# Kernel optimization log

Measured on AMD Instinct MI355X. Metric: run time of the kernel, lower is better.

## Reference

```python
import jax, jax.numpy as jnp
import numpy as np

N = 100000        # nodes
E = 1600000       # edges (avg degree 16)
F_IN = 128        # in_features
AH = 16           # attention_size
ALPHA = 0.2       # LeakyReLU negative slope


def setup_inputs() -> dict:
    key = jax.random.key(0)
    ks = jax.random.split(key, 10)
    xav = lambda k, shp, fan: jax.random.normal(k, shp, jnp.float32) * (1.414 * (2.0 / fan) ** 0.5)
    return {
        "input": jax.random.normal(ks[0], (N, F_IN), jnp.float32),
        "edges": jax.random.randint(ks[1], (2, E), 0, N, jnp.int32),
        "edge_factor": jax.random.normal(ks[2], (E,), jnp.float32),
        "adj_sparse_sum_rowwise": jnp.ones((N, 1), jnp.float32),
        "degree": jax.random.uniform(ks[3], (N,), jnp.float32) + 0.1,
        # Linear_2mini: in_features -> attention_hid
        "w_mini": xav(ks[4], (F_IN, AH), F_IN + AH),
        "b_mini": jnp.zeros((AH,), jnp.float32),
        "attention_bias": jnp.zeros((1, AH), jnp.float32),
        # linear_factor1: 3*AH -> AH ; linear_factor2: AH -> 1
        "lf1_w": xav(ks[5], (3 * AH, AH), 4 * AH),
        "lf1_b": jnp.zeros((AH,), jnp.float32),
        "lf2_w": xav(ks[6], (AH, 1), AH + 1),
        "lf2_b": jnp.zeros((1,), jnp.float32),
        "adj": 0,
        "iftrain": 0,
    }


def _edge_mlp(h_src, h_dst, h_diff, lf1_w, lf1_b, lf2_w, lf2_b):
    # [E, 3*AH] -> [E, AH] -> leaky_relu -> [E, 1] -> sigmoid -> [E]
    f = jnp.concatenate([h_src, h_dst, h_diff], axis=1)
    f = f @ lf1_w + lf1_b
    f = jax.nn.leaky_relu(f, ALPHA)
    f = f @ lf2_w + lf2_b
    return jax.nn.sigmoid(f[:, 0])


def reference(input, edges, edge_factor, adj_sparse_sum_rowwise, degree,
              w_mini, b_mini, attention_bias, lf1_w, lf1_b, lf2_w, lf2_b,
              adj, iftrain):
    n = input.shape[0]
    src, dst = edges[0], edges[1]

    # Linear_2mini projection [N, AH]
    new_h_mini = input @ w_mini + b_mini
    h_src = new_h_mini[src]                   # [E, AH]
    h_dst = new_h_mini[dst]                   # [E, AH]
    h_diff = jnp.abs(h_dst - h_src)           # [E, AH]

    # first edge MLP -> sigmoid factor per edge
    fc0 = _edge_mlp(h_src, h_dst, h_diff, lf1_w, lf1_b, lf2_w, lf2_b)  # [E]

    # row-wise MEAN of fc0 over edges grouped by source row (spmm reduce='mean')
    row_cnt = jax.ops.segment_sum(jnp.ones_like(fc0), src, num_segments=n)
    factor_res_1hop = jax.ops.segment_sum(fc0, src, num_segments=n) / jnp.maximum(row_cnt, 1.0)  # [N]

    factor_src = factor_res_1hop[src]         # [E]
    factor_dst = factor_res_1hop[dst]         # [E]

    # second edge MLP with attention bias added to endpoints
    fc1 = _edge_mlp(h_src + attention_bias, h_dst + attention_bias, h_diff,
                    lf1_w, lf1_b, lf2_w, lf2_b)  # [E]

    ef = factor_src * factor_dst * fc1        # new edge_factor [E]

    # row-wise SUM of edge factors (spmm with ones, reduce='sum')
    ef_row_sum = jax.ops.segment_sum(ef, src, num_segments=n)[:, None]  # [N,1]
    aggr_factor = ef_row_sum / adj_sparse_sum_rowwise                   # [N,1]

    deg = degree[:, None]                                               # [N,1]
    # sparse matmul: out[i] = sum_{e: src[e]=i} ef[e] * (input*deg)[dst[e]]
    msg = ef[:, None] * (input * deg)[dst]                              # [E, F]
    spmm = jax.ops.segment_sum(msg, src, num_segments=n)                # [N, F]

    final_h = spmm * deg + (1.0 - aggr_factor) * input
    return final_h, ef
```

## Files before the change

### kernel.cpp

```cpp
#include <hip/hip_runtime.h>
#include <math.h>

#define F_IN 128
#define AH 16
#define ALPHA 0.2f
#define NB_MAX 1024
#define TILE 2048
#define EPT 8
#define CAP 5120
#define PCAP 6144

typedef __attribute__((ext_vector_type(8))) short short8;
typedef __attribute__((ext_vector_type(4))) float f32x4;
typedef __attribute__((ext_vector_type(2))) float f32x2;

__device__ __forceinline__ unsigned f2bf_rn(float x) {
    unsigned u = __float_as_uint(x);
    return (u + 0x7fffu + ((u >> 16) & 1u)) >> 16;
}
#define LOF(u) __uint_as_float((u) << 16)
#define HIF(u) __uint_as_float((u) & 0xffff0000u)

#if __has_builtin(__builtin_amdgcn_cvt_pk_fp8_f32) && __has_builtin(__builtin_amdgcn_cvt_pk_f32_fp8)
__device__ __forceinline__ unsigned short fp8_pack2(float x, float y) {
    return (unsigned short)(__builtin_amdgcn_cvt_pk_fp8_f32(x, y, 0, false) & 0xffff);
}
__device__ __forceinline__ f32x2 fp8_unpack2(unsigned short u) {
    return __builtin_amdgcn_cvt_pk_f32_fp8((int)(unsigned)u, false);
}
#else
__device__ __forceinline__ unsigned fp8_enc1(float x) {
    unsigned u = __float_as_uint(x);
    const unsigned s = (u >> 24) & 0x80u;
    u &= 0x7fffffffu;
    if (u < 0x3C000000u) return s;
    if (u < 0x3C800000u) return s | 0x08u;
    const unsigned r = u + 0x7ffffu + ((u >> 20) & 1u);
    const unsigned e32 = r >> 23;
    return s | (((e32 - 120u) & 0xfu) << 3) | ((r >> 20) & 7u);
}
__device__ __forceinline__ unsigned short fp8_pack2(float x, float y) {
    return (unsigned short)(fp8_enc1(x) | (fp8_enc1(y) << 8));
}
__device__ __forceinline__ float fp8_dec1(unsigned b) {
    return __uint_as_float(((b & 0x80u) << 24) | ((b & 0x7fu) << 20)) * 0x1p120f;
}
__device__ __forceinline__ f32x2 fp8_unpack2(unsigned short u) {
    f32x2 r; r.x = fp8_dec1((unsigned)u & 0xffu); r.y = fp8_dec1((unsigned)u >> 8);
    return r;
}
#endif


__global__ void k_mini(const float* __restrict__ input,
                       const float* __restrict__ w,
                       const float* __restrict__ b,
                       const float* __restrict__ degree,
                       unsigned short* __restrict__ hb,
                       unsigned short* __restrict__ simf8, int n) {
    __shared__ float ws[F_IN * AH];
    __shared__ float rows[16][F_IN + 1];
    __shared__ float dgs[16];
    for (int i = threadIdx.x; i < F_IN * AH; i += blockDim.x) ws[i] = w[i];
    const int base = blockIdx.x * 16;
    for (int idx = threadIdx.x; idx < 16 * F_IN; idx += blockDim.x) {
        const int l = idx >> 7, f = idx & 127;
        const int node = base + l;
        rows[l][f] = (node < n) ? input[(size_t)node * F_IN + f] : 0.f;
    }
    if (threadIdx.x < 16) {
        const int node = base + threadIdx.x;
        dgs[threadIdx.x] = (node < n) ? degree[node] : 0.f;
    }
    __syncthreads();
    {
        const int l = threadIdx.x >> 4;
        const int j = threadIdx.x & 15;
        const int node = base + l;
        if (node < n) {
            float acc = b[j];
            #pragma unroll 8
            for (int f = 0; f < F_IN; ++f) acc += rows[l][f] * ws[f * AH + j];
            hb[(size_t)node * AH + j] = (unsigned short)f2bf_rn(acc);
        }
    }
    for (int idx = threadIdx.x; idx < 16 * 64; idx += blockDim.x) {
        const int l = idx >> 6, pr = idx & 63;
        const int node = base + l;
        if (node < n) {
            const float dg = dgs[l];
            simf8[(size_t)node * 64 + pr] =
                fp8_pack2(rows[l][2 * pr] * dg, rows[l][2 * pr + 1] * dg);
        }
    }
}

__global__ void k_binit(int* __restrict__ bucket_cur, int nb1,
                        const float* __restrict__ lf1_w, const float* __restrict__ ab,
                        float* __restrict__ Cj) {
    for (int b = threadIdx.x; b < nb1; b += blockDim.x) bucket_cur[b] = b * CAP;
    if (threadIdx.x < AH) {
        float c = 0.f;
        for (int k = 0; k < AH; ++k)
            c += ab[k] * (lf1_w[k * AH + threadIdx.x] + lf1_w[(AH + k) * AH + threadIdx.x]);
        Cj[threadIdx.x] = c;
    }
}

__global__ __launch_bounds__(256, 4)
void k_mlp_part1(const int* __restrict__ src, const int* __restrict__ dst,
                 const unsigned short* __restrict__ hb,
                 const float* __restrict__ lf1_w, const float* __restrict__ lf1_b,
                 const float* __restrict__ lf2_w, const float* __restrict__ lf2_b,
                 const float* __restrict__ Cj,
                 unsigned* __restrict__ fcb,
                 int* __restrict__ bucket_cur,
                 unsigned long long* __restrict__ rec, int e, int nb1) {
    __shared__ unsigned lds_fc[TILE];
    __shared__ int lhist[NB_MAX];
    __shared__ int lbase[NB_MAX];
    const int t0   = blockIdx.x * TILE;
    const int lane = threadIdx.x & 63;
    const int wv   = threadIdx.x >> 6;
    const int g    = lane >> 4;
    const int col  = lane & 15;
    for (int k = threadIdx.x; k < nb1; k += 256) lhist[k] = 0;

    short8 A1, A2;
    #pragma unroll
    for (int i = 0; i < 8; ++i) {
        A1[i] = (short)f2bf_rn(lf1_w[(8 * g + i) * AH + col]);
        A2[i] = (g < 2) ? (short)f2bf_rn(lf1_w[(32 + 8 * g + i) * AH + col]) : (short)0;
    }
    const f32x4 bias4 = *(const f32x4*)(lf1_b + 4 * g);
    const f32x4 cj4   = *(const f32x4*)(Cj + 4 * g);
    const f32x4 w24   = *(const f32x4*)(lf2_w + 4 * g);
    const float b2    = lf2_b[0];

    const int CPW = TILE / 64;
    for (int c = wv * CPW; c < (wv + 1) * CPW; ++c) {
        const int eidx = t0 + c * 16 + col;
        const bool ev  = (eidx < e);
        const int s = ev ? src[eidx] : 0;
        const int d = ev ? dst[eidx] : 0;
        const int rowi = (g < 2) ? s : d;
        const uint4 B1u = *(const uint4*)(hb + (size_t)rowi * AH + (g & 1) * 8);
        uint4 H;
        H.x = (unsigned)__shfl_xor((int)B1u.x, 32);
        H.y = (unsigned)__shfl_xor((int)B1u.y, 32);
        H.z = (unsigned)__shfl_xor((int)B1u.z, 32);
        H.w = (unsigned)__shfl_xor((int)B1u.w, 32);
        uint4 B2u;
        B2u.x = (f2bf_rn(fabsf(HIF(H.x) - HIF(B1u.x))) << 16) | f2bf_rn(fabsf(LOF(H.x) - LOF(B1u.x)));
        B2u.y = (f2bf_rn(fabsf(HIF(H.y) - HIF(B1u.y))) << 16) | f2bf_rn(fabsf(LOF(H.y) - LOF(B1u.y)));
        B2u.z = (f2bf_rn(fabsf(HIF(H.z) - HIF(B1u.z))) << 16) | f2bf_rn(fabsf(LOF(H.z) - LOF(B1u.z)));
        B2u.w = (f2bf_rn(fabsf(HIF(H.w) - HIF(B1u.w))) << 16) | f2bf_rn(fabsf(LOF(H.w) - LOF(B1u.w)));

        f32x4 acc = bias4;
        acc = __builtin_amdgcn_mfma_f32_16x16x32_bf16(A1, *(const short8*)&B1u, acc, 0, 0, 0);
        acc = __builtin_amdgcn_mfma_f32_16x16x32_bf16(A2, *(const short8*)&B2u, acc, 0, 0, 0);

        float p0 = 0.f, p1 = 0.f;
        #pragma unroll
        for (int r = 0; r < 4; ++r) {
            const float f  = acc[r];
            const float v0 = f > 0.f ? f : ALPHA * f;
            const float t  = f + cj4[r];
            const float v1 = t > 0.f ? t : ALPHA * t;
            p0 += w24[r] * v0;
            p1 += w24[r] * v1;
        }
        p0 += __shfl_xor(p0, 16); p1 += __shfl_xor(p1, 16);
        p0 += __shfl_xor(p0, 32); p1 += __shfl_xor(p1, 32);
        if (lane < 16) {
            const float fc0 = 1.f / (1.f + expf(-(p0 + b2)));
            const float fc1 = 1.f / (1.f + expf(-(p1 + b2)));
            lds_fc[c * 16 + col] = (f2bf_rn(fc1) << 16) | f2bf_rn(fc0);
        }
    }
    __syncthreads();
    int sv[EPT], rv[EPT];
    #pragma unroll
    for (int k = 0; k < EPT; ++k) {
        const int i = t0 + k * 256 + threadIdx.x;
        if (i < e) {
            const int s = src[i];
            sv[k] = s;
            rv[k] = atomicAdd(&lhist[s >> 8], 1);
        } else { sv[k] = -1; rv[k] = 0; }
    }
    __syncthreads();
    for (int k = threadIdx.x; k < nb1; k += 256) {
        const int c = lhist[k];
        lbase[k] = c ? atomicAdd(&bucket_cur[k], c) : 0;
    }
    __syncthreads();
    #pragma unroll
    for (int k = 0; k < EPT; ++k) {
        const int i = t0 + k * 256 + threadIdx.x;
        if (i < e) {
            const int s = sv[k];
            const unsigned fc = lds_fc[i - t0];
            fcb[i] = fc;
            const unsigned lo = ((unsigned)(s & 255) << 24) | (unsigned)dst[i];
            rec[lbase[s >> 8] + rv[k]] = ((unsigned long long)fc << 32) | lo;
        }
    }
}

__global__ void k_bscan(const int* __restrict__ bucket_cur, int* __restrict__ base,
                        int nb1, int e) {
    __shared__ int sh[1024];
    const int t = threadIdx.x;
    const int v = (t < nb1) ? (bucket_cur[t] - t * CAP) : 0;
    sh[t] = v; __syncthreads();
    for (int off = 1; off < 1024; off <<= 1) {
        const int x = (t >= off) ? sh[t - off] : 0;
        __syncthreads();
        sh[t] += x;
        __syncthreads();
    }
    if (t < nb1) base[t] = sh[t] - v;
    if (t == nb1) base[t] = e;
}

__global__ __launch_bounds__(256)
void k_part2(const int* __restrict__ bucket_cur, const int* __restrict__ bucket_base,
             const unsigned long long* __restrict__ rec,
             unsigned long long* __restrict__ rec2,
             int* __restrict__ row_end, int* __restrict__ cnt,
             float* __restrict__ factor, int n) {
    __shared__ unsigned long long lds[PCAP];
    __shared__ int lcnt[256];
    __shared__ int sh[256];
    __shared__ float lsum[256];
    const int b = blockIdx.x;
    const int start = b * CAP;
    const int count = bucket_cur[b] - start;
    const int out0  = bucket_base[b];
    lcnt[threadIdx.x] = 0;
    lsum[threadIdx.x] = 0.f;
    __syncthreads();
    for (int k = threadIdx.x; k < count; k += 256) {
        const unsigned long long r = rec[start + k];
        if (k < PCAP) lds[k] = r;
        const int off = (int)(((unsigned)r >> 24) & 255u);
        atomicAdd(&lcnt[off], 1);
        atomicAdd(&lsum[off], __uint_as_float(((unsigned)(r >> 32) & 0xffffu) << 16));
    }
    __syncthreads();
    const int v = lcnt[threadIdx.x];
    sh[threadIdx.x] = v; __syncthreads();
    for (int off = 1; off < 256; off <<= 1) {
        const int x = (threadIdx.x >= off) ? sh[threadIdx.x - off] : 0;
        __syncthreads();
        sh[threadIdx.x] += x;
        __syncthreads();
    }
    const int inc = sh[threadIdx.x];
    const int node = (b << 8) + threadIdx.x;
    if (node < n) {
        row_end[node] = out0 + inc;
        cnt[node] = v;
        factor[node] = lsum[threadIdx.x] / fmaxf((float)v, 1.f);
    }
    lcnt[threadIdx.x] = inc - v;
    __syncthreads();
    for (int k = threadIdx.x; k < count; k += 256) {
        const unsigned long long r = (k < PCAP) ? lds[k] : rec[start + k];
        const int off = (int)(((unsigned)r >> 24) & 255u);
        const int p = out0 + atomicAdd(&lcnt[off], 1);
        rec2[p] = r;
    }
}

__global__ void k_ef(const int* __restrict__ src, const int* __restrict__ dst,
                     const unsigned* __restrict__ fcb, const float* __restrict__ factor,
                     float* __restrict__ ef_out, int e) {
    const int i = blockIdx.x * blockDim.x + threadIdx.x;
    if (i < e) {
        const unsigned fb = fcb[i];
        ef_out[i] = factor[src[i]] * factor[dst[i]] *
                    __uint_as_float(fb & 0xffff0000u);
    }
}

__global__ void k_spmm_final(const int* __restrict__ row_end, const int* __restrict__ cnt,
                             const unsigned long long* __restrict__ rec,
                             const float* __restrict__ factor,
                             const unsigned short* __restrict__ simf8,
                             const float* __restrict__ input,
                             const float* __restrict__ degree,
                             const float* __restrict__ adj_row,
                             float* __restrict__ out_h, int n) {
    __shared__ float2 sh[256];
    const int wid  = (blockIdx.x * blockDim.x + threadIdx.x) >> 6;
    const int lane = threadIdx.x & 63;
    const int sbase = threadIdx.x & ~63;
    if (wid >= n) return;
    const int end = row_end[wid];
    const int beg = end - cnt[wid];
    const float fnode = factor[wid];
    float acc0 = 0.f, acc1 = 0.f, efl = 0.f;
    for (int base = beg; base < end; base += 64) {
        const int rem = end - base;
        const int mm = rem < 64 ? rem : 64;
        float ef = 0.f; int dl = 0;
        if (lane < mm) {
            const unsigned long long r = rec[base + lane];
            const int d = (int)((unsigned)r & 0xffffffu);
            const float fc1 = __uint_as_float((unsigned)(r >> 32) & 0xffff0000u);
            ef = fnode * factor[d] * fc1;
            dl = d;
        }
        efl += ef;
        sh[sbase + lane] = make_float2(ef, __int_as_float(dl));
        for (int j = 0; j < mm; j += 8) {
            float2 t0 = sh[sbase + j + 0];
            float2 t1 = sh[sbase + j + 1];
            float2 t2 = sh[sbase + j + 2];
            float2 t3 = sh[sbase + j + 3];
            float2 t4 = sh[sbase + j + 4];
            float2 t5 = sh[sbase + j + 5];
            float2 t6 = sh[sbase + j + 6];
            float2 t7 = sh[sbase + j + 7];
            const unsigned short u0 = simf8[(size_t)__float_as_int(t0.y) * 64 + lane];
            const unsigned short u1 = simf8[(size_t)__float_as_int(t1.y) * 64 + lane];
            const unsigned short u2 = simf8[(size_t)__float_as_int(t2.y) * 64 + lane];
            const unsigned short u3 = simf8[(size_t)__float_as_int(t3.y) * 64 + lane];
            const unsigned short u4 = simf8[(size_t)__float_as_int(t4.y) * 64 + lane];
            const unsigned short u5 = simf8[(size_t)__float_as_int(t5.y) * 64 + lane];
            const unsigned short u6 = simf8[(size_t)__float_as_int(t6.y) * 64 + lane];
            const unsigned short u7 = simf8[(size_t)__float_as_int(t7.y) * 64 + lane];
            const f32x2 v0 = fp8_unpack2(u0);
            const f32x2 v1 = fp8_unpack2(u1);
            const f32x2 v2 = fp8_unpack2(u2);
            const f32x2 v3 = fp8_unpack2(u3);
            const f32x2 v4 = fp8_unpack2(u4);
            const f32x2 v5 = fp8_unpack2(u5);
            const f32x2 v6 = fp8_unpack2(u6);
            const f32x2 v7 = fp8_unpack2(u7);
            acc0 += t0.x * v0.x; acc1 += t0.x * v0.y;
            acc0 += t1.x * v1.x; acc1 += t1.x * v1.y;
            acc0 += t2.x * v2.x; acc1 += t2.x * v2.y;
            acc0 += t3.x * v3.x; acc1 += t3.x * v3.y;
            acc0 += t4.x * v4.x; acc1 += t4.x * v4.y;
            acc0 += t5.x * v5.x; acc1 += t5.x * v5.y;
            acc0 += t6.x * v6.x; acc1 += t6.x * v6.y;
            acc0 += t7.x * v7.x; acc1 += t7.x * v7.y;
        }
    }
    for (int off = 32; off > 0; off >>= 1) efl += __shfl_xor(efl, off);
    const float aggr = efl / adj_row[wid];
    const float dg = degree[wid];
    const float2 inn = *(const float2*)(input + (size_t)wid * F_IN + 2 * lane);
    float2 o;
    o.x = acc0 * dg + (1.f - aggr) * inn.x;
    o.y = acc1 * dg + (1.f - aggr) * inn.y;
    *(float2*)(out_h + (size_t)wid * F_IN + 2 * lane) = o;
}

extern "C" void kernel_launch(void* const* d_in, const int* in_sizes, int n_in,
                              void* d_out, int out_size, void* d_ws, size_t ws_size,
                              hipStream_t stream) {
    const float* input   = (const float*)d_in[0];
    const int*   edges   = (const int*)  d_in[1];
    const float* adj_row = (const float*)d_in[3];
    const float* degree  = (const float*)d_in[4];
    const float* w_mini  = (const float*)d_in[5];
    const float* b_mini  = (const float*)d_in[6];
    const float* ab      = (const float*)d_in[7];
    const float* lf1_w   = (const float*)d_in[8];
    const float* lf1_b   = (const float*)d_in[9];
    const float* lf2_w   = (const float*)d_in[10];
    const float* lf2_b   = (const float*)d_in[11];

    const int N = in_sizes[0] / F_IN;
    const int E = in_sizes[1] / 2;
    const int NB1 = (N + 255) >> 8;
    const int* src = edges;
    const int* dst = edges + E;

    float* final_h = (float*)d_out;
    float* ef_out  = (float*)d_out + (size_t)N * F_IN;

    unsigned short* hb  = (unsigned short*)d_ws;
    unsigned* fcb  = (unsigned*)(hb + (size_t)N * AH);
    float* factor  = (float*)(fcb + E);
    int*   cnt     = (int*)(factor + N);
    int*   row_end = cnt + N;
    float* Cj      = (float*)(row_end + N);
    int*   bucket_base = (int*)(Cj + 16);
    int*   bucket_cur  = bucket_base + NB_MAX + 1;
    unsigned long long* rec =
        (unsigned long long*)((((uintptr_t)(bucket_cur + NB_MAX)) + 15) & ~(uintptr_t)15);
    unsigned long long* rec2 = rec + (size_t)NB1 * CAP;
    unsigned short* simf8 =
        (unsigned short*)((((uintptr_t)(rec2 + E)) + 255) & ~(uintptr_t)255);

    k_mini<<<(N + 15) / 16, 256, 0, stream>>>(input, w_mini, b_mini, degree, hb, simf8, N);
    k_binit<<<1, 512, 0, stream>>>(bucket_cur, NB1, lf1_w, ab, Cj);
    k_mlp_part1<<<(E + TILE - 1) / TILE, 256, 0, stream>>>(src, dst, hb,
                                                           lf1_w, lf1_b, lf2_w, lf2_b, Cj,
                                                           fcb, bucket_cur, rec, E, NB1);
    k_bscan<<<1, 1024, 0, stream>>>(bucket_cur, bucket_base, NB1, E);
    k_part2<<<NB1, 256, 0, stream>>>(bucket_cur, bucket_base, rec, rec2,
                                     row_end, cnt, factor, N);
    k_ef<<<(E + 255) / 256, 256, 0, stream>>>(src, dst, fcb, factor, ef_out, E);
    k_spmm_final<<<(N * 64 + 255) / 256, 256, 0, stream>>>(row_end, cnt, rec2, factor, simf8,
                                                           input, degree, adj_row, final_h, N);
}
```

Baseline: 205.8 us.

## Split edge MLP from bucket scatter into separate kernels with grid-stride MFMA loop

Un-fuses the MFMA edge-MLP from the bucketing/scatter stage. The MLP now runs as a persistent grid-stride kernel writing fc values straight to global memory. A separate kernel, with a doubled tile and elements per thread, builds the local histogram and scatters records, reading fc back from global. The aim is better MLP occupancy and fewer global bucket atomics, at the cost of an extra launch and an extra global round trip for fcb.

Result: faster. 201.2 us (-2.2%).

```diff
diff --git a/kernel.cpp b/kernel.cpp
--- a/kernel.cpp
+++ b/kernel.cpp
@@ -5,8 +5,8 @@
 #define AH 16
 #define ALPHA 0.2f
 #define NB_MAX 1024
-#define TILE 2048
-#define EPT 8
+#define TILE 4096
+#define EPT 16
 #define CAP 5120
 #define PCAP 6144
 
@@ -108,23 +108,15 @@
 }
 
 __global__ __launch_bounds__(256, 4)
-void k_mlp_part1(const int* __restrict__ src, const int* __restrict__ dst,
-                 const unsigned short* __restrict__ hb,
-                 const float* __restrict__ lf1_w, const float* __restrict__ lf1_b,
-                 const float* __restrict__ lf2_w, const float* __restrict__ lf2_b,
-                 const float* __restrict__ Cj,
-                 unsigned* __restrict__ fcb,
-                 int* __restrict__ bucket_cur,
-                 unsigned long long* __restrict__ rec, int e, int nb1) {
-    __shared__ unsigned lds_fc[TILE];
-    __shared__ int lhist[NB_MAX];
-    __shared__ int lbase[NB_MAX];
-    const int t0   = blockIdx.x * TILE;
+void k_mlp_mfma(const int* __restrict__ src, const int* __restrict__ dst,
+                const unsigned short* __restrict__ hb,
+                const float* __restrict__ lf1_w, const float* __restrict__ lf1_b,
+                const float* __restrict__ lf2_w, const float* __restrict__ lf2_b,
+                const float* __restrict__ Cj,
+                unsigned* __restrict__ fcb, int e) {
     const int lane = threadIdx.x & 63;
-    const int wv   = threadIdx.x >> 6;
     const int g    = lane >> 4;
     const int col  = lane & 15;
-    for (int k = threadIdx.x; k < nb1; k += 256) lhist[k] = 0;
 
     short8 A1, A2;
     #pragma unroll
@@ -137,9 +129,11 @@
     const f32x4 w24   = *(const f32x4*)(lf2_w + 4 * g);
     const float b2    = lf2_b[0];
 
-    const int CPW = TILE / 64;
-    for (int c = wv * CPW; c < (wv + 1) * CPW; ++c) {
-        const int eidx = t0 + c * 16 + col;
+    const int wid    = (blockIdx.x * blockDim.x + threadIdx.x) >> 6;
+    const int nw     = (gridDim.x * blockDim.x) >> 6;
+    const int nbatch = (e + 15) >> 4;
+    for (int bt = wid; bt < nbatch; bt += nw) {
+        const int eidx = bt * 16 + col;
         const bool ev  = (eidx < e);
         const int s = ev ? src[eidx] : 0;
         const int d = ev ? dst[eidx] : 0;
@@ -172,12 +166,23 @@
         }
         p0 += __shfl_xor(p0, 16); p1 += __shfl_xor(p1, 16);
         p0 += __shfl_xor(p0, 32); p1 += __shfl_xor(p1, 32);
-        if (lane < 16) {
+        if (lane < 16 && ev) {
             const float fc0 = 1.f / (1.f + expf(-(p0 + b2)));
             const float fc1 = 1.f / (1.f + expf(-(p1 + b2)));
-            lds_fc[c * 16 + col] = (f2bf_rn(fc1) << 16) | f2bf_rn(fc0);
-        }
-    }
+            fcb[eidx] = (f2bf_rn(fc1) << 16) | f2bf_rn(fc0);
+        }
+    }
+}
+
+__global__ __launch_bounds__(256)
+void k_part1(const int* __restrict__ src, const int* __restrict__ dst,
+             const unsigned* __restrict__ fcb,
+             int* __restrict__ bucket_cur,
+             unsigned long long* __restrict__ rec, int e, int nb1) {
+    __shared__ int lhist[NB_MAX];
+    __shared__ int lbase[NB_MAX];
+    const int t0 = blockIdx.x * TILE;
+    for (int k = threadIdx.x; k < nb1; k += 256) lhist[k] = 0;
     __syncthreads();
     int sv[EPT], rv[EPT];
     #pragma unroll
@@ -200,10 +205,8 @@
         const int i = t0 + k * 256 + threadIdx.x;
         if (i < e) {
             const int s = sv[k];
-            const unsigned fc = lds_fc[i - t0];
-            fcb[i] = fc;
             const unsigned lo = ((unsigned)(s & 255) << 24) | (unsigned)dst[i];
-            rec[lbase[s >> 8] + rv[k]] = ((unsigned long long)fc << 32) | lo;
+            rec[lbase[s >> 8] + rv[k]] = ((unsigned long long)fcb[i] << 32) | lo;
         }
     }
 }
@@ -400,9 +403,11 @@
 
     k_mini<<<(N + 15) / 16, 256, 0, stream>>>(input, w_mini, b_mini, degree, hb, simf8, N);
     k_binit<<<1, 512, 0, stream>>>(bucket_cur, NB1, lf1_w, ab, Cj);
-    k_mlp_part1<<<(E + TILE - 1) / TILE, 256, 0, stream>>>(src, dst, hb,
-                                                           lf1_w, lf1_b, lf2_w, lf2_b, Cj,
-                                                           fcb, bucket_cur, rec, E, NB1);
+    k_mlp_mfma<<<2048, 256, 0, stream>>>(src, dst, hb,
+                                         lf1_w, lf1_b, lf2_w, lf2_b, Cj,
+                                         fcb, E);
+    k_part1<<<(E + TILE - 1) / TILE, 256, 0, stream>>>(src, dst, fcb,
+                                                       bucket_cur, rec, E, NB1);
     k_bscan<<<1, 1024, 0, stream>>>(bucket_cur, bucket_base, NB1, E);
     k_part2<<<NB1, 256, 0, stream>>>(bucket_cur, bucket_base, rec, rec2,
                                      row_end, cnt, factor, N);
```
